# Performance work log

Measured on AMD Instinct MI355X. Metric: run time of the kernel, lower is better.

Reference implementation:

```python
import jax, jax.numpy as jnp
import numpy as np

N_PTS = 65536
N_VERTS = 6890
N_JOINTS = 24


def build_rotation(q):
    # q: [N,4] unnormalized quaternion (r, x, y, z) -> [N,3,3] rotation matrix
    q = q / jnp.linalg.norm(q, axis=-1, keepdims=True)
    r, x, y, z = q[:, 0], q[:, 1], q[:, 2], q[:, 3]
    R = jnp.stack([
        1 - 2 * (y * y + z * z), 2 * (x * y - r * z), 2 * (x * z + r * y),
        2 * (x * y + r * z), 1 - 2 * (x * x + z * z), 2 * (y * z - r * x),
        2 * (x * z - r * y), 2 * (y * z + r * x), 1 - 2 * (x * x + y * y),
    ], axis=-1).reshape(-1, 3, 3)
    return R


def setup_inputs() -> dict:
    key = jax.random.key(0)
    k1, k2, k3, k4, k5 = jax.random.split(key, 5)
    xyz = jax.random.normal(k1, (N_PTS, 3), dtype=jnp.float32)
    rotation = jax.random.normal(k2, (N_PTS, 4), dtype=jnp.float32)
    smpl_verts = jax.random.normal(k3, (N_VERTS, 3), dtype=jnp.float32)
    skinning_weights = jax.random.uniform(k4, (N_VERTS, N_JOINTS), dtype=jnp.float32)
    # row-normalize like real LBS weights
    skinning_weights = skinning_weights / jnp.sum(skinning_weights, axis=-1, keepdims=True)
    bone_transforms = jax.random.normal(k5, (N_JOINTS, 4, 4), dtype=jnp.float32)
    return {"xyz": xyz, "rotation": rotation, "smpl_verts": smpl_verts,
            "skinning_weights": skinning_weights, "bone_transforms": bone_transforms}


def reference(xyz, rotation, smpl_verts, skinning_weights, bone_transforms):
    # --- 1-NN brute-force search (knn_points with K=1) ---
    d2 = (jnp.sum(xyz * xyz, axis=-1, keepdims=True)
          - 2.0 * (xyz @ smpl_verts.T)
          + jnp.sum(smpl_verts * smpl_verts, axis=-1)[None, :])
    p_idx = jnp.argmin(d2, axis=-1)                      # [N]

    # --- skinning-weight gather ---
    pts_W = skinning_weights[p_idx]                      # [N, 24]

    # --- LBS: blend bone transforms ---
    T_fwd = (pts_W @ bone_transforms.reshape(-1, 16)).reshape(-1, 4, 4)  # [N,4,4]

    # --- transform points (homogeneous) ---
    x_bar = jnp.einsum('nij,nj->ni', T_fwd[:, :3, :3], xyz) + T_fwd[:, :3, 3]  # [N,3]

    # --- rotate covariance rotations ---
    rotation_hat = build_rotation(rotation)              # [N,3,3]
    rotation_bar = jnp.einsum('nij,njk->nik', T_fwd[:, :3, :3], rotation_hat)  # [N,3,3]

    return (x_bar, rotation_bar, T_fwd)
```

## Files before the change

### kernel.cpp

```cpp
#include <hip/hip_runtime.h>
#include <math.h>

#define NPTS 65536
#define NV 6890
#define NT 432
#define NTA 440
#define NJ 24
#define NBINS 4096
#define VSPLIT 8
#define WIN 16
#define PTS_PER_BLK 64
#define NBLK (NPTS / PTS_PER_BLK)

typedef double f64x4 __attribute__((ext_vector_type(4)));

__device__ __forceinline__ unsigned mspread(unsigned v) {
    return (v & 1u) | ((v & 2u) << 2) | ((v & 4u) << 4) | ((v & 8u) << 6);
}
__device__ __forceinline__ unsigned morton12(float x, float y, float z) {
    int qx = (int)floorf((x + 4.0f) * 2.0f); qx = qx < 0 ? 0 : (qx > 15 ? 15 : qx);
    int qy = (int)floorf((y + 4.0f) * 2.0f); qy = qy < 0 ? 0 : (qy > 15 ? 15 : qy);
    int qz = (int)floorf((z + 4.0f) * 2.0f); qz = qz < 0 ? 0 : (qz > 15 ? 15 : qz);
    return mspread((unsigned)qx) | (mspread((unsigned)qy) << 1) | (mspread((unsigned)qz) << 2);
}

__global__ void hist2_k(const float* __restrict__ xyz, const float* __restrict__ verts,
                        unsigned* __restrict__ pbins, unsigned* __restrict__ prank,
                        unsigned* __restrict__ vbins, unsigned* __restrict__ vrank) {
    int i = blockIdx.x * blockDim.x + threadIdx.x;
    if (i < NPTS) {
        unsigned c = morton12(xyz[3 * i], xyz[3 * i + 1], xyz[3 * i + 2]);
        prank[i] = atomicAdd(&pbins[c], 1u);
    } else {
        int j = i - NPTS;
        if (j < NV) {
            unsigned c = morton12(verts[3 * j], verts[3 * j + 1], verts[3 * j + 2]);
            vrank[j] = atomicAdd(&vbins[c], 1u);
        }
    }
}

__global__ void prefix_k(const unsigned* __restrict__ pb, const unsigned* __restrict__ vb,
                         unsigned* __restrict__ ps, unsigned* __restrict__ vs) {
    __shared__ unsigned s[NBINS];
    const int tid = threadIdx.x;
    for (int pass = 0; pass < 2; ++pass) {
        const unsigned* in = pass ? vb : pb;
        unsigned* outp = pass ? vs : ps;
        for (int j = tid; j < NBINS; j += 1024) s[j] = in[j];
        __syncthreads();
        for (int off = 1; off < NBINS; off <<= 1) {
            unsigned v[4];
            #pragma unroll
            for (int q = 0; q < 4; ++q) {
                int j = tid + q * 1024;
                v[q] = (j >= off) ? s[j - off] : 0u;
            }
            __syncthreads();
            #pragma unroll
            for (int q = 0; q < 4; ++q) s[tid + q * 1024] += v[q];
            __syncthreads();
        }
        for (int j = tid; j < NBINS; j += 1024) outp[j + 1] = s[j];
        if (tid == 0) outp[0] = 0;
        __syncthreads();
    }
}

__global__ void scatter2_k(const float* __restrict__ xyz, const float* __restrict__ verts,
                           const unsigned* __restrict__ pstart, const unsigned* __restrict__ prank,
                           const unsigned* __restrict__ vstart, const unsigned* __restrict__ vrank,
                           int* __restrict__ pord, int* __restrict__ vord) {
    int i = blockIdx.x * blockDim.x + threadIdx.x;
    if (i < NPTS) {
        unsigned c = morton12(xyz[3 * i], xyz[3 * i + 1], xyz[3 * i + 2]);
        pord[pstart[c] + prank[i]] = i;
    } else {
        int j = i - NPTS;
        if (j < NV) {
            unsigned c = morton12(verts[3 * j], verts[3 * j + 1], verts[3 * j + 2]);
            vord[vstart[c] + vrank[j]] = j;
        }
    }
}

__global__ void prep_frags_k(const float* __restrict__ verts, const int* __restrict__ vord,
                             double* __restrict__ bf) {
    int e = blockIdx.x * blockDim.x + threadIdx.x;
    if (e >= NTA * 64) return;
    int l = e & 63;
    int t = e >> 6;
    int pos = t * 16 + (l & 15);
    int k = l >> 4;
    double val;
    if (pos < NV) {
        int j = vord[pos];
        if (k < 3) {
            val = (double)verts[3 * j + k];
        } else {
            double x = (double)verts[3 * j + 0];
            double y = (double)verts[3 * j + 1];
            double z = (double)verts[3 * j + 2];
            val = x * x + y * y + z * z;
        }
    } else {
        val = (k == 3) ? 1e300 : 0.0;
    }
    bf[e] = val;
}

__global__ void tilebb_k(const float* __restrict__ verts, const int* __restrict__ vord,
                         float4* __restrict__ tbb) {
    int t = blockIdx.x * blockDim.x + threadIdx.x;
    if (t >= NTA) return;
    if (t * 16 >= NV) { tbb[t] = make_float4(1e30f, 1e30f, 1e30f, 0.0f); return; }
    float mnx = 1e30f, mny = 1e30f, mnz = 1e30f;
    float mxx = -1e30f, mxy = -1e30f, mxz = -1e30f;
    for (int c = 0; c < 16; ++c) {
        int pos = t * 16 + c;
        if (pos >= NV) break;
        int j = vord[pos];
        float x = verts[3 * j], y = verts[3 * j + 1], z = verts[3 * j + 2];
        mnx = fminf(mnx, x); mxx = fmaxf(mxx, x);
        mny = fminf(mny, y); mxy = fmaxf(mxy, y);
        mnz = fminf(mnz, z); mxz = fmaxf(mxz, z);
    }
    float cx = (mnx + mxx) * 0.5f, cy = (mny + mxy) * 0.5f, cz = (mnz + mxz) * 0.5f;
    float r2 = 0.0f;
    for (int c = 0; c < 16; ++c) {
        int pos = t * 16 + c;
        if (pos >= NV) break;
        int j = vord[pos];
        float dx = verts[3 * j] - cx, dy = verts[3 * j + 1] - cy, dz = verts[3 * j + 2] - cz;
        r2 = fmaxf(r2, dx * dx + dy * dy + dz * dz);
    }
    float r = sqrtf(r2) * 1.0002f + 1e-5f;
    tbb[t] = make_float4(cx, cy, cz, r);
}

__device__ __forceinline__ void packmin(double& m, double d, unsigned orv) {
    unsigned long long u = __double_as_longlong(d);
    u = (u & ~0x1FFFULL) | (unsigned long long)orv;
    double t = __longlong_as_double(u);
    asm("v_min_f64 %0, %0, %1" : "+v"(m) : "v"(t));
}

__device__ __forceinline__ void epilogue(int i, int bi,
                                         const float* __restrict__ xyz,
                                         const float* __restrict__ rot,
                                         const float* __restrict__ sw,
                                         const float* __restrict__ bt,
                                         float* __restrict__ out) {
    const float xf = xyz[3 * i + 0];
    const float yf = xyz[3 * i + 1];
    const float zf = xyz[3 * i + 2];

    const float* W = &sw[bi * NJ];
    float Tm[16];
    #pragma unroll
    for (int q = 0; q < 16; ++q) Tm[q] = 0.0f;
    #pragma unroll
    for (int kk = 0; kk < NJ; ++kk) {
        float w = W[kk];
        #pragma unroll
        for (int q = 0; q < 16; ++q) Tm[q] = fmaf(w, bt[16 * kk + q], Tm[q]);
    }

    float xb0 = Tm[0] * xf + Tm[1] * yf + Tm[2]  * zf + Tm[3];
    float xb1 = Tm[4] * xf + Tm[5] * yf + Tm[6]  * zf + Tm[7];
    float xb2 = Tm[8] * xf + Tm[9] * yf + Tm[10] * zf + Tm[11];

    float qr = rot[4 * i + 0];
    float qx = rot[4 * i + 1];
    float qy = rot[4 * i + 2];
    float qz = rot[4 * i + 3];
    float inv = 1.0f / sqrtf(qr * qr + qx * qx + qy * qy + qz * qz);
    qr *= inv; qx *= inv; qy *= inv; qz *= inv;

    float Rh[9];
    Rh[0] = 1.0f - 2.0f * (qy * qy + qz * qz);
    Rh[1] = 2.0f * (qx * qy - qr * qz);
    Rh[2] = 2.0f * (qx * qz + qr * qy);
    Rh[3] = 2.0f * (qx * qy + qr * qz);
    Rh[4] = 1.0f - 2.0f * (qx * qx + qz * qz);
    Rh[5] = 2.0f * (qy * qz - qr * qx);
    Rh[6] = 2.0f * (qx * qz - qr * qy);
    Rh[7] = 2.0f * (qy * qz + qr * qx);
    Rh[8] = 1.0f - 2.0f * (qx * qx + qy * qy);

    float RB[9];
    #pragma unroll
    for (int rr2 = 0; rr2 < 3; ++rr2) {
        #pragma unroll
        for (int cc = 0; cc < 3; ++cc) {
            RB[3 * rr2 + cc] = Tm[4 * rr2 + 0] * Rh[cc]
                             + Tm[4 * rr2 + 1] * Rh[3 + cc]
                             + Tm[4 * rr2 + 2] * Rh[6 + cc];
        }
    }

    out[3 * i + 0] = xb0;
    out[3 * i + 1] = xb1;
    out[3 * i + 2] = xb2;
    float* ob = out + 3 * NPTS + 9 * i;
    #pragma unroll
    for (int q = 0; q < 9; ++q) ob[q] = RB[q];
    float* ot = out + 12 * NPTS + 16 * i;
    #pragma unroll
    for (int q = 0; q < 16; ++q) ot[q] = Tm[q];
}

__launch_bounds__(512)
__global__ void smplnn_scan(const float* __restrict__ xyz,
                            const float* __restrict__ rot,
                            const double* __restrict__ bf,
                            const float* __restrict__ sw,
                            const float* __restrict__ bt,
                            const int* __restrict__ pord,
                            const int* __restrict__ vord,
                            const float4* __restrict__ tbb,
                            const unsigned* __restrict__ vstart,
                            float* __restrict__ out) {
    __shared__ float4 stbb[NTA];
    __shared__ double smin2[VSPLIT][PTS_PER_BLK];
    __shared__ unsigned short slist[448];
    __shared__ int scount;

    const int tid  = threadIdx.x;
    const int lane = tid & 63;
    const int wave = tid >> 6;
    const int r = lane & 15;
    const int k = lane >> 4;
    const int pbase = blockIdx.x * PTS_PER_BLK;

    for (int j = tid; j < NTA; j += 512) stbb[j] = tbb[j];
    if (tid == 0) scount = 0;

    const int o0 = pord[pbase + r];
    const int o1 = pord[pbase + 16 + r];
    const int o2 = pord[pbase + 32 + r];
    const int o3 = pord[pbase + 48 + r];
    double a0 = (k == 3) ? 1.0 : -2.0 * (double)xyz[3 * o0 + k];
    double a1 = (k == 3) ? 1.0 : -2.0 * (double)xyz[3 * o1 + k];
    double a2 = (k == 3) ? 1.0 : -2.0 * (double)xyz[3 * o2 + k];
    double a3 = (k == 3) ? 1.0 : -2.0 * (double)xyz[3 * o3 + k];

    const int om = pord[pbase + lane];
    const float px = xyz[3 * om], py = xyz[3 * om + 1], pz = xyz[3 * om + 2];
    const double pn = (double)px * px + (double)py * py + (double)pz * pz;

    float bxmin = px, bxmax = px, bymin = py, bymax = py, bzmin = pz, bzmax = pz;
    #pragma unroll
    for (int s = 1; s < 64; s <<= 1) {
        bxmin = fminf(bxmin, __shfl_xor(bxmin, s));
        bxmax = fmaxf(bxmax, __shfl_xor(bxmax, s));
        bymin = fminf(bymin, __shfl_xor(bymin, s));
        bymax = fmaxf(bymax, __shfl_xor(bymax, s));
        bzmin = fminf(bzmin, __shfl_xor(bzmin, s));
        bzmax = fmaxf(bzmax, __shfl_xor(bzmax, s));
    }

    const f64x4 zero = {0.0, 0.0, 0.0, 0.0};

    double ar  = (k == 3) ? (double)r : 0.0;
    double one = (k == 3) ? 1.0 : 0.0;
    f64x4 drow = __builtin_amdgcn_mfma_f64_16x16x4f64(ar, one, zero, 0, 0, 0);
    f64x4 dcol = __builtin_amdgcn_mfma_f64_16x16x4f64(one, ar, zero, 0, 0, 0);
    int rowid[4];
    unsigned colb[4];
    #pragma unroll
    for (int v = 0; v < 4; ++v) { rowid[v] = (int)drow[v]; colb[v] = (unsigned)(int)dcol[v]; }

    double m0[4], m1[4], m2[4], m3[4];
    #pragma unroll
    for (int v = 0; v < 4; ++v) { m0[v] = 1e301; m1[v] = 1e301; m2[v] = 1e301; m3[v] = 1e301; }

#define PROCESS(T, B) do {                                                        \
        unsigned tb_ = ((unsigned)(T)) << 4;                                      \
        f64x4 d0 = __builtin_amdgcn_mfma_f64_16x16x4f64(a0, (B), zero, 0, 0, 0);  \
        f64x4 d1 = __builtin_amdgcn_mfma_f64_16x16x4f64(a1, (B), zero, 0, 0, 0);  \
        f64x4 d2 = __builtin_amdgcn_mfma_f64_16x16x4f64(a2, (B), zero, 0, 0, 0);  \
        f64x4 d3 = __builtin_amdgcn_mfma_f64_16x16x4f64(a3, (B), zero, 0, 0, 0);  \
        unsigned q0_ = tb_ | colb[0], q1_ = tb_ | colb[1];                        \
        unsigned q2_ = tb_ | colb[2], q3_ = tb_ | colb[3];                        \
        packmin(m0[0], d0[0], q0_); packmin(m0[1], d0[1], q1_);                   \
        packmin(m0[2], d0[2], q2_); packmin(m0[3], d0[3], q3_);                   \
        packmin(m1[0], d1[0], q0_); packmin(m1[1], d1[1], q1_);                   \
        packmin(m1[2], d1[2], q2_); packmin(m1[3], d1[3], q3_);                   \
        packmin(m2[0], d2[0], q0_); packmin(m2[1], d2[1], q1_);                   \
        packmin(m2[2], d2[2], q2_); packmin(m2[3], d2[3], q3_);                   \
        packmin(m3[0], d3[0], q0_); packmin(m3[1], d3[1], q1_);                   \
        packmin(m3[2], d3[2], q2_); packmin(m3[3], d3[3], q3_);                   \
    } while (0)

    unsigned bc = morton12((bxmin + bxmax) * 0.5f, (bymin + bymax) * 0.5f,
                           (bzmin + bzmax) * 0.5f);
    int tw0 = ((int)vstart[bc] >> 4) - WIN / 2;
    if (tw0 < 0) tw0 = 0;
    if (tw0 > NT - WIN) tw0 = NT - WIN;
    tw0 = __builtin_amdgcn_readfirstlane(tw0);

    {
        int ta = tw0 + 2 * wave;
        double ba = bf[(size_t)ta * 64 + lane];
        double bb2 = bf[(size_t)(ta + 1) * 64 + lane];
        PROCESS(ta, ba);
        PROCESS(ta + 1, bb2);
    }

    auto publish = [&]() {
        double val = 0.0;
        #pragma unroll
        for (int f = 0; f < 4; ++f) {
            #pragma unroll
            for (int v = 0; v < 4; ++v) {
                double q = (f == 0) ? m0[v] : (f == 1) ? m1[v] : (f == 2) ? m2[v] : m3[v];
                #pragma unroll
                for (int s = 1; s < 16; s <<= 1) q = fmin(q, __shfl_xor(q, s, 16));
                if ((lane & 15) == f * 4 + v) val = q;
            }
        }
        smin2[wave][((lane & 15) >> 2) * 16 + rowid[lane & 3]] = val;
    };

    publish();
    __syncthreads();

    double bp_ = smin2[0][lane];
    #pragma unroll
    for (int w = 1; w < VSPLIT; ++w) bp_ = fmin(bp_, smin2[w][lane]);
    double d2 = bp_ + pn;
    if (d2 < 0.0) d2 = 0.0;
    #pragma unroll
    for (int s = 1; s < 64; s <<= 1) d2 = fmax(d2, __shfl_xor(d2, s));
    const float sU = sqrtf((float)(d2 * 1.000002 + 1e-9)) + 1e-6f;
    __syncthreads();

    if (tid < NT) {
        const int t = tid;
        float4 s0 = stbb[t];
        float dx = fmaxf(0.0f, fmaxf(s0.x - bxmax, bxmin - s0.x));
        float dy = fmaxf(0.0f, fmaxf(s0.y - bymax, bymin - s0.y));
        float dz = fmaxf(0.0f, fmaxf(s0.z - bzmax, bzmin - s0.z));
        float gap = sqrtf(dx * dx + dy * dy + dz * dz) - s0.w;
        bool keep = (gap <= sU) && (t < tw0 || t >= tw0 + WIN);
        if (keep) {
            int p = atomicAdd(&scount, 1);
            slist[p] = (unsigned short)t;
        }
    }
    __syncthreads();

    const int M = scount;
    const int Mp = (M + VSPLIT - 1) & ~(VSPLIT - 1);
    if (tid >= M && tid < Mp) slist[tid] = NT;
    __syncthreads();

    {
        const int nit = Mp / VSPLIT;
        if (nit > 0) {
            int icur = wave;
            int tcur = slist[icur];
            double bcur = bf[(size_t)tcur * 64 + lane];
            for (int j = 0; j < nit; ++j) {
                int inext = icur + VSPLIT;
                int tnext = (j + 1 < nit) ? (int)slist[inext] : NT;
                double bnext = bf[(size_t)tnext * 64 + lane];
                PROCESS(tcur, bcur);
                icur = inext; tcur = tnext; bcur = bnext;
            }
        }
    }

    publish();
    __syncthreads();

    if (wave != 0) return;

    double best = smin2[0][lane];
    #pragma unroll
    for (int w = 1; w < VSPLIT; ++w) best = fmin(best, smin2[w][lane]);
    const int bpos = (int)(__double_as_longlong(best) & 0x1FFFULL);
    const int bi = vord[bpos];
    const int oi = pord[pbase + lane];
    epilogue(oi, bi, xyz, rot, sw, bt, out);
#undef PROCESS
}

extern "C" void kernel_launch(void* const* d_in, const int* in_sizes, int n_in,
                              void* d_out, int out_size, void* d_ws, size_t ws_size,
                              hipStream_t stream) {
    const float* xyz   = (const float*)d_in[0];
    const float* rot   = (const float*)d_in[1];
    const float* verts = (const float*)d_in[2];
    const float* sw    = (const float*)d_in[3];
    const float* bt    = (const float*)d_in[4];
    float* out = (float*)d_out;

    double*   bfrag  = (double*)d_ws;
    float4*   tbb    = (float4*)(bfrag + NTA * 64);
    int*      pord   = (int*)(tbb + NTA);
    int*      vord   = pord + NPTS;
    unsigned* prank  = (unsigned*)(vord + 6912);
    unsigned* vrank  = prank + NPTS;
    unsigned* pbins  = vrank + 6912;
    unsigned* vbins  = pbins + NBINS;
    unsigned* pstart = vbins + NBINS;
    unsigned* vstart = pstart + NBINS + 4;

    hipMemsetAsync(pbins, 0, 2 * NBINS * sizeof(unsigned), stream);

    hist2_k<<<(NPTS + NV + 255) / 256, 256, 0, stream>>>(xyz, verts, pbins, prank, vbins, vrank);
    prefix_k<<<1, 1024, 0, stream>>>(pbins, vbins, pstart, vstart);
    scatter2_k<<<(NPTS + NV + 255) / 256, 256, 0, stream>>>(xyz, verts, pstart, prank,
                                                            vstart, vrank, pord, vord);
    prep_frags_k<<<(NTA * 64) / 256, 256, 0, stream>>>(verts, vord, bfrag);
    tilebb_k<<<(NTA + 63) / 64, 64, 0, stream>>>(verts, vord, tbb);

    smplnn_scan<<<NBLK, 512, 0, stream>>>(xyz, rot, bfrag, sw, bt,
                                          pord, vord, tbb, vstart, out);
}
```

Before: 135.1 us.

## Cull vertex tiles per point instead of per block bounding box; fuse tilebb into prep

Tile culling now tests each vertex tile's bounding sphere against every point's own nearest-distance upper bound, rather than one block-wide AABB with the block's worst-case radius. This gives a tighter candidate list, so fewer tiles go through the fp64 exact scan. The test costs 64 shared-memory iterations per tile thread. The separate tile bounding-box kernel is also merged into prep_frags_k to save one launch.

```diff
diff --git a/kernel.cpp b/kernel.cpp
--- a/kernel.cpp
+++ b/kernel.cpp
@@ -85,57 +85,55 @@
 }
 
 __global__ void prep_frags_k(const float* __restrict__ verts, const int* __restrict__ vord,
-                             double* __restrict__ bf) {
+                             double* __restrict__ bf, float4* __restrict__ tbb) {
     int e = blockIdx.x * blockDim.x + threadIdx.x;
-    if (e >= NTA * 64) return;
-    int l = e & 63;
-    int t = e >> 6;
-    int pos = t * 16 + (l & 15);
-    int k = l >> 4;
-    double val;
-    if (pos < NV) {
-        int j = vord[pos];
-        if (k < 3) {
-            val = (double)verts[3 * j + k];
+    if (e < NTA * 64) {
+        int l = e & 63;
+        int t = e >> 6;
+        int pos = t * 16 + (l & 15);
+        int k = l >> 4;
+        double val;
+        if (pos < NV) {
+            int j = vord[pos];
+            if (k < 3) {
+                val = (double)verts[3 * j + k];
+            } else {
+                double x = (double)verts[3 * j + 0];
+                double y = (double)verts[3 * j + 1];
+                double z = (double)verts[3 * j + 2];
+                val = x * x + y * y + z * z;
+            }
         } else {
-            double x = (double)verts[3 * j + 0];
-            double y = (double)verts[3 * j + 1];
-            double z = (double)verts[3 * j + 2];
-            val = x * x + y * y + z * z;
-        }
-    } else {
-        val = (k == 3) ? 1e300 : 0.0;
-    }
-    bf[e] = val;
-}
-
-__global__ void tilebb_k(const float* __restrict__ verts, const int* __restrict__ vord,
-                         float4* __restrict__ tbb) {
-    int t = blockIdx.x * blockDim.x + threadIdx.x;
-    if (t >= NTA) return;
-    if (t * 16 >= NV) { tbb[t] = make_float4(1e30f, 1e30f, 1e30f, 0.0f); return; }
-    float mnx = 1e30f, mny = 1e30f, mnz = 1e30f;
-    float mxx = -1e30f, mxy = -1e30f, mxz = -1e30f;
-    for (int c = 0; c < 16; ++c) {
-        int pos = t * 16 + c;
-        if (pos >= NV) break;
-        int j = vord[pos];
-        float x = verts[3 * j], y = verts[3 * j + 1], z = verts[3 * j + 2];
-        mnx = fminf(mnx, x); mxx = fmaxf(mxx, x);
-        mny = fminf(mny, y); mxy = fmaxf(mxy, y);
-        mnz = fminf(mnz, z); mxz = fmaxf(mxz, z);
-    }
-    float cx = (mnx + mxx) * 0.5f, cy = (mny + mxy) * 0.5f, cz = (mnz + mxz) * 0.5f;
-    float r2 = 0.0f;
-    for (int c = 0; c < 16; ++c) {
-        int pos = t * 16 + c;
-        if (pos >= NV) break;
-        int j = vord[pos];
-        float dx = verts[3 * j] - cx, dy = verts[3 * j + 1] - cy, dz = verts[3 * j + 2] - cz;
-        r2 = fmaxf(r2, dx * dx + dy * dy + dz * dz);
-    }
-    float r = sqrtf(r2) * 1.0002f + 1e-5f;
-    tbb[t] = make_float4(cx, cy, cz, r);
+            val = (k == 3) ? 1e300 : 0.0;
+        }
+        bf[e] = val;
+    }
+    if (e < NTA) {
+        int t = e;
+        if (t * 16 >= NV) { tbb[t] = make_float4(1e30f, 1e30f, 1e30f, 0.0f); return; }
+        float mnx = 1e30f, mny = 1e30f, mnz = 1e30f;
+        float mxx = -1e30f, mxy = -1e30f, mxz = -1e30f;
+        for (int c = 0; c < 16; ++c) {
+            int pos = t * 16 + c;
+            if (pos >= NV) break;
+            int j = vord[pos];
+            float x = verts[3 * j], y = verts[3 * j + 1], z = verts[3 * j + 2];
+            mnx = fminf(mnx, x); mxx = fmaxf(mxx, x);
+            mny = fminf(mny, y); mxy = fmaxf(mxy, y);
+            mnz = fminf(mnz, z); mxz = fmaxf(mxz, z);
+        }
+        float cx = (mnx + mxx) * 0.5f, cy = (mny + mxy) * 0.5f, cz = (mnz + mxz) * 0.5f;
+        float r2 = 0.0f;
+        for (int c = 0; c < 16; ++c) {
+            int pos = t * 16 + c;
+            if (pos >= NV) break;
+            int j = vord[pos];
+            float dx = verts[3 * j] - cx, dy = verts[3 * j + 1] - cy, dz = verts[3 * j + 2] - cz;
+            r2 = fmaxf(r2, dx * dx + dy * dy + dz * dz);
+        }
+        float r = sqrtf(r2) * 1.0002f + 1e-5f;
+        tbb[t] = make_float4(cx, cy, cz, r);
+    }
 }
 
 __device__ __forceinline__ void packmin(double& m, double d, unsigned orv) {
@@ -223,6 +221,7 @@
                             float* __restrict__ out) {
     __shared__ float4 stbb[NTA];
     __shared__ double smin2[VSPLIT][PTS_PER_BLK];
+    __shared__ float4 spts[PTS_PER_BLK];
     __shared__ unsigned short slist[448];
     __shared__ int scount;
 
@@ -329,24 +328,30 @@
     double bp_ = smin2[0][lane];
     #pragma unroll
     for (int w = 1; w < VSPLIT; ++w) bp_ = fmin(bp_, smin2[w][lane]);
-    double d2 = bp_ + pn;
-    if (d2 < 0.0) d2 = 0.0;
-    #pragma unroll
-    for (int s = 1; s < 64; s <<= 1) d2 = fmax(d2, __shfl_xor(d2, s));
-    const float sU = sqrtf((float)(d2 * 1.000002 + 1e-9)) + 1e-6f;
+    double d2p = bp_ + pn;
+    if (d2p < 0.0) d2p = 0.0;
+    const float sup = sqrtf((float)(d2p * 1.00001 + 1e-8)) + 1e-4f;
+    if (wave == 0) spts[lane] = make_float4(px, py, pz, sup);
     __syncthreads();
 
     if (tid < NT) {
         const int t = tid;
         float4 s0 = stbb[t];
-        float dx = fmaxf(0.0f, fmaxf(s0.x - bxmax, bxmin - s0.x));
-        float dy = fmaxf(0.0f, fmaxf(s0.y - bymax, bymin - s0.y));
-        float dz = fmaxf(0.0f, fmaxf(s0.z - bzmax, bzmin - s0.z));
-        float gap = sqrtf(dx * dx + dy * dy + dz * dz) - s0.w;
-        bool keep = (gap <= sU) && (t < tw0 || t >= tw0 + WIN);
+        const float rt = s0.w;
+        const float r2t = rt * rt;
+        float acc = 1.0f;
+        #pragma unroll 4
+        for (int p = 0; p < PTS_PER_BLK; ++p) {
+            float4 q = spts[p];
+            float dx = q.x - s0.x, dy = q.y - s0.y, dz = q.z - s0.z;
+            float dist2 = fmaf(dx, dx, fmaf(dy, dy, dz * dz));
+            float rhs = fmaf(2.0f * rt, q.w, fmaf(q.w, q.w, r2t));
+            acc = fminf(acc, dist2 - rhs);
+        }
+        bool keep = (acc <= 0.0f) && (t < tw0 || t >= tw0 + WIN);
         if (keep) {
-            int p = atomicAdd(&scount, 1);
-            slist[p] = (unsigned short)t;
+            int p2 = atomicAdd(&scount, 1);
+            slist[p2] = (unsigned short)t;
         }
     }
     __syncthreads();
@@ -414,8 +419,7 @@
     prefix_k<<<1, 1024, 0, stream>>>(pbins, vbins, pstart, vstart);
     scatter2_k<<<(NPTS + NV + 255) / 256, 256, 0, stream>>>(xyz, verts, pstart, prank,
                                                             vstart, vrank, pord, vord);
-    prep_frags_k<<<(NTA * 64) / 256, 256, 0, stream>>>(verts, vord, bfrag);
-    tilebb_k<<<(NTA + 63) / 64, 64, 0, stream>>>(verts, vord, tbb);
+    prep_frags_k<<<(NTA * 64 + 255) / 256, 256, 0, stream>>>(verts, vord, bfrag, tbb);
 
     smplnn_scan<<<NBLK, 512, 0, stream>>>(xyz, rot, bfrag, sw, bt,
                                           pord, vord, tbb, vstart, out);
```

Result: faster. 119.1 us (-11.8%).
